# Performance work log

Measured on AMD Instinct MI355X. Metric: run time of the kernel, lower is better.

## Reference

```python
import jax, jax.numpy as jnp
import numpy as np

H = 25  # blstm_hidden_size


def _lstm_bidir(x_tbf, w_ih, w_hh, b_ih, b_hh):
    """One bidirectional LSTM layer (PyTorch gate order i,f,g,o).
    x_tbf: (T,B,F); w_ih: (2,4H,F); w_hh: (2,4H,H); b_ih/b_hh: (2,4H).
    Returns (T,B,2H) with [fwd, bwd] concatenated on features."""
    T, B, _ = x_tbf.shape
    Hd = w_hh.shape[2]

    def run(d, reverse):
        # precompute input contribution for all timesteps (one big GEMM)
        xg = jnp.einsum('tbf,gf->tbg', x_tbf, w_ih[d]) + b_ih[d] + b_hh[d]
        whh_t = w_hh[d].T  # (H,4H)

        def step(carry, g):
            h, c = carry
            g = g + h @ whh_t
            i, f, gg, o = jnp.split(g, 4, axis=-1)
            c = jax.nn.sigmoid(f) * c + jax.nn.sigmoid(i) * jnp.tanh(gg)
            h = jax.nn.sigmoid(o) * jnp.tanh(c)
            return (h, c), h

        init = (jnp.zeros((B, Hd), x_tbf.dtype), jnp.zeros((B, Hd), x_tbf.dtype))
        _, hs = jax.lax.scan(step, init, xg, reverse=reverse)
        return hs  # (T,B,H), time-aligned with input for both directions

    return jnp.concatenate([run(0, False), run(1, True)], axis=-1)


def setup_inputs() -> dict:
    key = jax.random.key(0)
    ks = jax.random.split(key, 16)
    B, T, F = 64, 3000, 314
    s = 1.0 / np.sqrt(H)  # PyTorch LSTM default init bound

    def u(k, shape, a):
        return jax.random.uniform(k, shape, jnp.float32, -a, a)

    inp = {'x': jax.random.normal(ks[0], (B, T, F), jnp.float32)}
    in_sizes = [F, 2 * H, 2 * H]
    for l in range(3):
        inp[f'w_ih_l{l}'] = u(ks[1 + 4 * l], (2, 4 * H, in_sizes[l]), s)
        inp[f'w_hh_l{l}'] = u(ks[2 + 4 * l], (2, 4 * H, H), s)
        inp[f'b_ih_l{l}'] = u(ks[3 + 4 * l], (2, 4 * H), s)
        inp[f'b_hh_l{l}'] = u(ks[4 + 4 * l], (2, 4 * H), s)
    inp['fc_w'] = u(ks[13], (3, 2 * H), 0.1)  # reset_params: uniform(-0.1,0.1)
    inp['fc_b'] = u(ks[14], (3,), 0.1)
    return inp


def reference(x, w_ih_l0, w_hh_l0, b_ih_l0, b_hh_l0,
              w_ih_l1, w_hh_l1, b_ih_l1, b_hh_l1,
              w_ih_l2, w_hh_l2, b_ih_l2, b_hh_l2,
              fc_w, fc_b):
    h = jnp.swapaxes(x, 0, 1)  # (T,B,F) for scan over time
    h = _lstm_bidir(h, w_ih_l0, w_hh_l0, b_ih_l0, b_hh_l0)
    h = _lstm_bidir(h, w_ih_l1, w_hh_l1, b_ih_l1, b_hh_l1)
    h = _lstm_bidir(h, w_ih_l2, w_hh_l2, b_ih_l2, b_hh_l2)
    out = h @ fc_w.T + fc_b  # (T,B,3)
    return jnp.swapaxes(out, 0, 1)  # (B,T,3)
```

## Files before the change

### kernel.cpp

```cpp
#include <hip/hip_runtime.h>

#define T_LEN 3000
#define BATCH 64
#define G4 100

#define TS 200
#define NCH 15
#define WARM 64

#define LOG2E 1.442695041f

typedef float v2f __attribute__((ext_vector_type(2)));

template <int MODE>
__global__ __launch_bounds__(256) void gemm_xg(
    const float* __restrict__ in, const float* __restrict__ w_ih,
    const float* __restrict__ b_ih, const float* __restrict__ b_hh,
    float* __restrict__ xg, int K) {
  __shared__ float lds_x[64][33];
  __shared__ __align__(16) float lds_w[100][32];

  const int tid = threadIdx.x;
  const int dir = blockIdx.y;
  const int r0 = blockIdx.x * 64;
  const int lane = tid & 63;
  const int wv = tid >> 6;
  const int c0 = wv * 25;
  const float* wbase = w_ih + (size_t)dir * G4 * K;

  v2f acc2[25];
#pragma unroll
  for (int c = 0; c < 25; ++c) {
    float bias = b_ih[dir * G4 + c0 + c] + b_hh[dir * G4 + c0 + c];
    acc2[c] = (v2f){bias, 0.f};
  }

  for (int k0 = 0; k0 < K; k0 += 32) {
    const int kw = min(32, K - k0);
#pragma unroll
    for (int i = 0; i < 8; ++i) {
      int e = tid + i * 256;
      int rr = e >> 5, kk = e & 31;
      int grow = r0 + rr;
      const float* rp;
      if (MODE == 0) {
        int tt = grow >> 6, bb = grow & 63;
        rp = in + ((size_t)bb * T_LEN + tt) * K;
      } else {
        rp = in + (size_t)grow * K;
      }
      lds_x[rr][kk] = (kk < kw) ? rp[k0 + kk] : 0.f;
    }
#pragma unroll
    for (int i = 0; i < 13; ++i) {
      int e = tid + i * 256;
      if (e < 3200) {
        int j = e >> 5, kk = e & 31;
        lds_w[j][kk] = (kk < kw) ? wbase[(size_t)j * K + k0 + kk] : 0.f;
      }
    }
    __syncthreads();
#pragma unroll
    for (int k4 = 0; k4 < 8; ++k4) {
      float xv0 = lds_x[lane][k4 * 4 + 0];
      float xv1 = lds_x[lane][k4 * 4 + 1];
      float xv2 = lds_x[lane][k4 * 4 + 2];
      float xv3 = lds_x[lane][k4 * 4 + 3];
      v2f x01 = (v2f){xv0, xv1};
      v2f x23 = (v2f){xv2, xv3};
#pragma unroll
      for (int c = 0; c < 25; ++c) {
        float4 w4 = *(const float4*)&lds_w[c0 + c][k4 * 4];
        v2f wlo = (v2f){w4.x, w4.y};
        v2f whi = (v2f){w4.z, w4.w};
        acc2[c] = __builtin_elementwise_fma(x01, wlo, acc2[c]);
        acc2[c] = __builtin_elementwise_fma(x23, whi, acc2[c]);
      }
    }
    __syncthreads();
  }
  const float sc = (wv == 2) ? 2.f * LOG2E : -LOG2E;
  const int row = r0 + lane;
  float* orow = xg + ((size_t)dir * T_LEN * BATCH + row) * G4 + c0;
#pragma unroll
  for (int c = 0; c < 25; ++c) orow[c] = (acc2[c].x + acc2[c].y) * sc;
}

__device__ __forceinline__ float frcp(float x) { return __builtin_amdgcn_rcpf(x); }
__device__ __forceinline__ float exp2f_fast(float x) {
  float r;
  asm("v_exp_f32 %0, %1" : "=v"(r) : "v"(x));
  return r;
}

typedef int v2i __attribute__((ext_vector_type(2)));

__global__ __launch_bounds__(512)
__attribute__((amdgpu_waves_per_eu(2, 2)))
void lstm_scan(
    const float* __restrict__ xg,
    const float* __restrict__ w_hh,
    float* __restrict__ hout) {
  const int wid = threadIdx.x >> 6;
  const int lane = threadIdx.x & 63;
  const int g = blockIdx.x * 8 + wid;
  const int seq = g / NCH;
  const int ch = g - seq * NCH;
  const int dir = seq & 1;
  const int b = seq >> 1;
  const bool isC = lane >= 32;
  const int nn = lane & 31;
  const int n = (nn < 25) ? nn : 24;
  const bool writer = isC && (nn < 25);
  const int qA = n + (isC ? 25 : 0);
  const int qB = qA + 50;

  __shared__ __align__(16) float h_lds[8][28];

  v2i tr = __builtin_amdgcn_permlane32_swap(lane, lane, 0, 0);
  const bool pick0 = (tr[0] == (lane ^ 32));

  const float sA = -LOG2E;
  const float sB = isC ? -LOG2E : 2.f * LOG2E;
  const float* wb = w_hh + (size_t)dir * G4 * 25;
  float wA[25], wB[25];
#pragma unroll
  for (int k = 0; k < 25; ++k) {
    wA[k] = wb[qA * 25 + k] * sA;
    wB[k] = wb[qB * 25 + k] * sB;
  }
#pragma unroll
  for (int k = 0; k < 25; ++k) {
    asm volatile("" : "+v"(wA[k]), "+v"(wB[k]));
  }

  if (lane < 28) h_lds[wid][lane] = 0.f;
  asm volatile("s_waitcnt lgkmcnt(0)" ::: "memory");

  float c = 0.f;

  const int W = (ch == 0) ? 0 : WARM;
  const int s0 = ch * TS - W;
  const int t0 = dir ? (T_LEN - 1 - s0) : s0;

  const ptrdiff_t rowstr = dir ? -(BATCH * G4) : (BATCH * G4);
  const float* pfp = xg + (size_t)dir * T_LEN * BATCH * G4 +
                     (size_t)t0 * (BATCH * G4) + (size_t)b * G4;

  auto refill = [&](float (&dst)[4][2]) {
    const float* r = pfp;
#pragma unroll
    for (int d = 0; d < 4; ++d) {
      dst[d][0] = r[qA];
      dst[d][1] = r[qB];
      r += rowstr;
    }
    pfp = r;
  };

  auto step = [&](float (&p)[2]) -> float {
    float hv[28];
#pragma unroll
    for (int q = 0; q < 7; ++q)
      *(float4*)&hv[4 * q] = *(const float4*)&h_lds[wid][4 * q];
    float pA = p[0], pB = p[1];
#pragma unroll
    for (int k = 0; k < 25; ++k) {
      pA = fmaf(wA[k], hv[k], pA);
      pB = fmaf(wB[k], hv[k], pB);
    }
    float aA = frcp(1.f + exp2f_fast(pA));
    float rB = frcp(1.f + exp2f_fast(pB));
    float bg = isC ? rB : fmaf(-2.f, rB, 1.f);
    float u = aA * bg;
    int ui = __float_as_int(u);
    v2i r = __builtin_amdgcn_permlane32_swap(ui, ui, 0, 0);
    float uu = __int_as_float(pick0 ? r[0] : r[1]);
    c = fmaf(aA, c, uu);
    float tc = fmaf(-2.f, frcp(1.f + exp2f_fast(2.f * LOG2E * c)), 1.f);
    float hn = bg * tc;
    if (writer) h_lds[wid][n] = hn;
    asm volatile("s_waitcnt lgkmcnt(0)" ::: "memory");
    return hn;
  };

  float pf[2][4][2];
  refill(pf[0]);
  refill(pf[1]);

  for (int it = 0; it < (W >> 3); ++it) {
#pragma unroll
    for (int d = 0; d < 4; ++d) step(pf[0][d]);
    refill(pf[0]);
#pragma unroll
    for (int d = 0; d < 4; ++d) step(pf[1][d]);
    refill(pf[1]);
  }

  const int tm = dir ? (T_LEN - 1 - ch * TS) : (ch * TS);
  const ptrdiff_t hstr = dir ? -(BATCH * 50) : (BATCH * 50);
  float* hp = hout + (size_t)tm * (BATCH * 50) + (size_t)b * 50 + dir * 25 + n;

  for (int it = 0; it < TS / 8; ++it) {
    float hb[8];
#pragma unroll
    for (int d = 0; d < 4; ++d) hb[d] = step(pf[0][d]);
    refill(pf[0]);
#pragma unroll
    for (int d = 0; d < 4; ++d) hb[4 + d] = step(pf[1][d]);
    refill(pf[1]);
    if (writer) {
#pragma unroll
      for (int d = 0; d < 8; ++d) hp[(ptrdiff_t)d * hstr] = hb[d];
    }
    hp += 8 * hstr;
  }
}

__global__ __launch_bounds__(256) void fc_kernel(
    const float* __restrict__ h, const float* __restrict__ fc_w,
    const float* __restrict__ fc_b, float* __restrict__ out) {
  int row = blockIdx.x * 256 + threadIdx.x;
  if (row >= T_LEN * BATCH) return;
  int t = row >> 6, b = row & 63;
  const float* hr = h + (size_t)row * 50;
  float a0 = fc_b[0], a1 = fc_b[1], a2 = fc_b[2];
#pragma unroll
  for (int j = 0; j < 50; ++j) {
    float v = hr[j];
    a0 = fmaf(v, fc_w[j], a0);
    a1 = fmaf(v, fc_w[50 + j], a1);
    a2 = fmaf(v, fc_w[100 + j], a2);
  }
  float* op = out + ((size_t)b * T_LEN + t) * 3;
  op[0] = a0; op[1] = a1; op[2] = a2;
}

extern "C" void kernel_launch(void* const* d_in, const int* in_sizes, int n_in,
                              void* d_out, int out_size, void* d_ws, size_t ws_size,
                              hipStream_t stream) {
  const float* x = (const float*)d_in[0];
  const float* w_ih[3] = {(const float*)d_in[1], (const float*)d_in[5], (const float*)d_in[9]};
  const float* w_hh[3] = {(const float*)d_in[2], (const float*)d_in[6], (const float*)d_in[10]};
  const float* b_ih[3] = {(const float*)d_in[3], (const float*)d_in[7], (const float*)d_in[11]};
  const float* b_hh[3] = {(const float*)d_in[4], (const float*)d_in[8], (const float*)d_in[12]};
  const float* fc_w = (const float*)d_in[13];
  const float* fc_b = (const float*)d_in[14];
  float* out = (float*)d_out;

  float* xg = (float*)d_ws;
  float* hA = xg + (size_t)2 * T_LEN * BATCH * G4;
  float* hB = hA + (size_t)T_LEN * BATCH * 50;

  dim3 gg(T_LEN * BATCH / 64, 2), gb(256);
  dim3 sg(240), sb(512);

  hipLaunchKernelGGL((gemm_xg<0>), gg, gb, 0, stream, x, w_ih[0], b_ih[0], b_hh[0], xg, 314);
  hipLaunchKernelGGL(lstm_scan, sg, sb, 0, stream, xg, w_hh[0], hA);
  hipLaunchKernelGGL((gemm_xg<1>), gg, gb, 0, stream, hA, w_ih[1], b_ih[1], b_hh[1], xg, 50);
  hipLaunchKernelGGL(lstm_scan, sg, sb, 0, stream, xg, w_hh[1], hB);
  hipLaunchKernelGGL((gemm_xg<1>), gg, gb, 0, stream, hB, w_ih[2], b_ih[2], b_hh[2], xg, 50);
  hipLaunchKernelGGL(lstm_scan, sg, sb, 0, stream, xg, w_hh[2], hA);
  hipLaunchKernelGGL(fc_kernel, dim3(T_LEN * BATCH / 256), dim3(256), 0, stream, hA, fc_w, fc_b, out);
}
```

Baseline: 1.345 ms.

## Keep input weights resident in LDS and loop persistent tiles with prefetch

The input-projection GEMM now loads the whole per-direction w_ih matrix into LDS once per block. Each block then walks several consecutive 64-row tiles instead of reloading weight chunks for every tile. The activation tile is double-buffered in LDS, and the next chunk's global loads are held in registers while the current chunk is computed, with one barrier per chunk. The cost is very large LDS use for layer 0 (about 145 KB), which allows one block per CU across a grid of 250 blocks and may limit latency hiding.

```diff
diff --git a/kernel.cpp b/kernel.cpp
--- a/kernel.cpp
+++ b/kernel.cpp
@@ -12,36 +12,44 @@
 
 typedef float v2f __attribute__((ext_vector_type(2)));
 
-template <int MODE>
+template <int MODE, int K, int NT>
 __global__ __launch_bounds__(256) void gemm_xg(
     const float* __restrict__ in, const float* __restrict__ w_ih,
     const float* __restrict__ b_ih, const float* __restrict__ b_hh,
-    float* __restrict__ xg, int K) {
-  __shared__ float lds_x[64][33];
-  __shared__ __align__(16) float lds_w[100][32];
+    float* __restrict__ xg) {
+  constexpr int KP = (K + 31) & ~31;
+  constexpr int NCHUNK = KP / 32;
+  __shared__ __align__(16) float lds_w[100][KP];
+  __shared__ float lds_x[2][64][33];
 
   const int tid = threadIdx.x;
   const int dir = blockIdx.y;
-  const int r0 = blockIdx.x * 64;
   const int lane = tid & 63;
   const int wv = tid >> 6;
   const int c0 = wv * 25;
   const float* wbase = w_ih + (size_t)dir * G4 * K;
 
-  v2f acc2[25];
-#pragma unroll
-  for (int c = 0; c < 25; ++c) {
-    float bias = b_ih[dir * G4 + c0 + c] + b_hh[dir * G4 + c0 + c];
-    acc2[c] = (v2f){bias, 0.f};
-  }
-
-  for (int k0 = 0; k0 < K; k0 += 32) {
-    const int kw = min(32, K - k0);
-#pragma unroll
-    for (int i = 0; i < 8; ++i) {
-      int e = tid + i * 256;
-      int rr = e >> 5, kk = e & 31;
-      int grow = r0 + rr;
+  for (int e = tid; e < 100 * KP; e += 256) {
+    int j = e / KP, kk = e - j * KP;
+    lds_w[j][kk] = (kk < K) ? wbase[(size_t)j * K + kk] : 0.f;
+  }
+
+  float bias25[25];
+#pragma unroll
+  for (int c = 0; c < 25; ++c)
+    bias25[c] = b_ih[dir * G4 + c0 + c] + b_hh[dir * G4 + c0 + c];
+  const float sc = (wv == 2) ? 2.f * LOG2E : -LOG2E;
+
+  const int t0 = blockIdx.x * NT;
+
+  float2 xreg[4];
+  auto issue = [&](int tile, int k0) {
+#pragma unroll
+    for (int i = 0; i < 4; ++i) {
+      int e = i * 256 + tid;
+      int rr = e >> 4;
+      int kp = (e & 15) * 2;
+      int grow = tile * 64 + rr;
       const float* rp;
       if (MODE == 0) {
         int tt = grow >> 6, bb = grow & 63;
@@ -49,41 +57,63 @@
       } else {
         rp = in + (size_t)grow * K;
       }
-      lds_x[rr][kk] = (kk < kw) ? rp[k0 + kk] : 0.f;
-    }
-#pragma unroll
-    for (int i = 0; i < 13; ++i) {
-      int e = tid + i * 256;
-      if (e < 3200) {
-        int j = e >> 5, kk = e & 31;
-        lds_w[j][kk] = (kk < kw) ? wbase[(size_t)j * K + k0 + kk] : 0.f;
+      int kc = min(k0 + kp, K - 2);
+      xreg[i] = *(const float2*)(rp + kc);
+    }
+  };
+  auto commit = [&](int p) {
+#pragma unroll
+    for (int i = 0; i < 4; ++i) {
+      int e = i * 256 + tid;
+      int rr = e >> 4;
+      int kp = (e & 15) * 2;
+      lds_x[p][rr][kp] = xreg[i].x;
+      lds_x[p][rr][kp + 1] = xreg[i].y;
+    }
+  };
+
+  issue(t0, 0);
+  asm volatile("s_waitcnt lgkmcnt(0)" ::: "memory");
+  __builtin_amdgcn_s_barrier();
+
+  int p = 0;
+  for (int it = 0; it < NT; ++it) {
+    const int tile = t0 + it;
+    v2f acc2[25];
+#pragma unroll
+    for (int c = 0; c < 25; ++c) acc2[c] = (v2f){bias25[c], 0.f};
+
+    for (int kc = 0; kc < NCHUNK; ++kc) {
+      commit(p);
+      if (kc + 1 < NCHUNK) issue(tile, (kc + 1) * 32);
+      else if (it + 1 < NT) issue(tile + 1, 0);
+      asm volatile("s_waitcnt lgkmcnt(0)" ::: "memory");
+      __builtin_amdgcn_s_barrier();
+      const int kb = kc * 32;
+#pragma unroll
+      for (int k4 = 0; k4 < 8; ++k4) {
+        float xv0 = lds_x[p][lane][k4 * 4 + 0];
+        float xv1 = lds_x[p][lane][k4 * 4 + 1];
+        float xv2 = lds_x[p][lane][k4 * 4 + 2];
+        float xv3 = lds_x[p][lane][k4 * 4 + 3];
+        v2f x01 = (v2f){xv0, xv1};
+        v2f x23 = (v2f){xv2, xv3};
+#pragma unroll
+        for (int c = 0; c < 25; ++c) {
+          float4 w4 = *(const float4*)&lds_w[c0 + c][kb + k4 * 4];
+          v2f wlo = (v2f){w4.x, w4.y};
+          v2f whi = (v2f){w4.z, w4.w};
+          acc2[c] = __builtin_elementwise_fma(x01, wlo, acc2[c]);
+          acc2[c] = __builtin_elementwise_fma(x23, whi, acc2[c]);
+        }
       }
-    }
-    __syncthreads();
-#pragma unroll
-    for (int k4 = 0; k4 < 8; ++k4) {
-      float xv0 = lds_x[lane][k4 * 4 + 0];
-      float xv1 = lds_x[lane][k4 * 4 + 1];
-      float xv2 = lds_x[lane][k4 * 4 + 2];
-      float xv3 = lds_x[lane][k4 * 4 + 3];
-      v2f x01 = (v2f){xv0, xv1};
-      v2f x23 = (v2f){xv2, xv3};
-#pragma unroll
-      for (int c = 0; c < 25; ++c) {
-        float4 w4 = *(const float4*)&lds_w[c0 + c][k4 * 4];
-        v2f wlo = (v2f){w4.x, w4.y};
-        v2f whi = (v2f){w4.z, w4.w};
-        acc2[c] = __builtin_elementwise_fma(x01, wlo, acc2[c]);
-        acc2[c] = __builtin_elementwise_fma(x23, whi, acc2[c]);
-      }
-    }
-    __syncthreads();
-  }
-  const float sc = (wv == 2) ? 2.f * LOG2E : -LOG2E;
-  const int row = r0 + lane;
-  float* orow = xg + ((size_t)dir * T_LEN * BATCH + row) * G4 + c0;
-#pragma unroll
-  for (int c = 0; c < 25; ++c) orow[c] = (acc2[c].x + acc2[c].y) * sc;
+      p ^= 1;
+    }
+    const int grow = tile * 64 + lane;
+    float* orow = xg + ((size_t)dir * T_LEN * BATCH + grow) * G4 + c0;
+#pragma unroll
+    for (int c = 0; c < 25; ++c) orow[c] = (acc2[c].x + acc2[c].y) * sc;
+  }
 }
 
 __device__ __forceinline__ float frcp(float x) { return __builtin_amdgcn_rcpf(x); }
@@ -252,14 +282,17 @@
   float* hA = xg + (size_t)2 * T_LEN * BATCH * G4;
   float* hB = hA + (size_t)T_LEN * BATCH * 50;
 
-  dim3 gg(T_LEN * BATCH / 64, 2), gb(256);
   dim3 sg(240), sb(512);
 
-  hipLaunchKernelGGL((gemm_xg<0>), gg, gb, 0, stream, x, w_ih[0], b_ih[0], b_hh[0], xg, 314);
+  hipLaunchKernelGGL((gemm_xg<0, 314, 24>), dim3(125, 2), dim3(256), 0, stream,
+                     x, w_ih[0], b_ih[0], b_hh[0], xg);
   hipLaunchKernelGGL(lstm_scan, sg, sb, 0, stream, xg, w_hh[0], hA);
-  hipLaunchKernelGGL((gemm_xg<1>), gg, gb, 0, stream, hA, w_ih[1], b_ih[1], b_hh[1], xg, 50);
+  hipLaunchKernelGGL((gemm_xg<1, 50, 8>), dim3(375, 2), dim3(256), 0, stream,
+                     hA, w_ih[1], b_ih[1], b_hh[1], xg);
   hipLaunchKernelGGL(lstm_scan, sg, sb, 0, stream, xg, w_hh[1], hB);
-  hipLaunchKernelGGL((gemm_xg<1>), gg, gb, 0, stream, hB, w_ih[2], b_ih[2], b_hh[2], xg, 50);
+  hipLaunchKernelGGL((gemm_xg<1, 50, 8>), dim3(375, 2), dim3(256), 0, stream,
+                     hB, w_ih[2], b_ih[2], b_hh[2], xg);
   hipLaunchKernelGGL(lstm_scan, sg, sb, 0, stream, xg, w_hh[2], hA);
-  hipLaunchKernelGGL(fc_kernel, dim3(T_LEN * BATCH / 256), dim3(256), 0, stream, hA, fc_w, fc_b, out);
-}
+  hipLaunchKernelGGL(fc_kernel, dim3(T_LEN * BATCH / 256), dim3(256), 0, stream,
+                     hA, fc_w, fc_b, out);
+}
```

Result: faster. 1.248 ms (-7.2%).
